# Kernel optimization log

Measured on AMD Instinct MI355X. Metric: run time of the kernel, lower is better.

## Reference

```python
import jax, jax.numpy as jnp
import numpy as np

L = 2          # loopnum
BS = 64        # batch
T = 512        # tracklength
EC = 1024      # ecnum
CA1 = 1024     # ca1num
CA3 = 1024     # ca3num
ACT = 2        # actnum
TS = 0.1
SIGMA = 5.0    # ca3sigma


def setup_inputs() -> dict:
    key = jax.random.key(0)
    ks = jax.random.split(key, 10)
    return {
        "cue_ec3input": jax.random.normal(ks[0], (BS, T, EC), dtype=jnp.float32),
        "ec3_last": jax.random.uniform(ks[1], (L, BS, EC), dtype=jnp.float32),
        "ec5_last": jax.random.uniform(ks[2], (L, BS, EC), dtype=jnp.float32),
        "ca1_last": jax.random.uniform(ks[3], (L, BS, CA1), dtype=jnp.float32),
        # per-loop parameters, stacked on leading loop axis (mirrors nn.ModuleList)
        "wca3ca1": jax.random.uniform(ks[4], (L, CA3, CA1), dtype=jnp.float32) * 0.01,
        "wec3ca1": jax.random.normal(ks[5], (L, EC, CA1), dtype=jnp.float32) * 0.03,   # ~xavier scale
        "wca1ec5": jax.random.normal(ks[6], (L, CA1, EC), dtype=jnp.float32) * 0.03,
        "ca1bias": jnp.zeros((L, CA1), dtype=jnp.float32),
        "ec5bias": jnp.zeros((L, EC), dtype=jnp.float32),
        # interLayer i: nn.Linear(ca1num, ecnum) -> weight (EC, CA1), bias (EC,)
        "inter_w": jax.random.normal(ks[7], (L, EC, CA1), dtype=jnp.float32) * 0.02,
        "inter_b": jnp.zeros((L, EC), dtype=jnp.float32),
        "wca1act": jax.random.normal(ks[8], (CA1, ACT), dtype=jnp.float32) * 0.03,
        "actbias": jnp.zeros((ACT,), dtype=jnp.float32),
    }


def reference(cue_ec3input, ec3_last, ec5_last, ca1_last,
              wca3ca1, wec3ca1, wca1ec5, ca1bias, ec5bias,
              inter_w, inter_b, wca1act, actbias):
    ca3center = jnp.linspace(0.0, float(T), CA3)          # (CA3,)
    positions = jnp.arange(T, dtype=jnp.float32)          # (T,)
    cue_t = jnp.swapaxes(cue_ec3input, 0, 1)              # (T, BS, EC)

    def step(carry, xin):
        ec3, ec5, ca1 = carry                             # each (L, BS, dim)
        x, cue_x = xin                                    # scalar, (BS, EC)
        ca3 = jnp.exp(-(ca3center - x) ** 2 / (2.0 * SIGMA ** 2))  # (CA3,)
        ec3input = cue_x
        new_ec3, new_ec5, new_ca1 = [], [], []
        for i in range(L):                                # fixed, structurally distinct loops
            ca1_i = jax.nn.relu(
                jax.nn.sigmoid(10.0 * (ca3 @ wca3ca1[i] - 0.5))           # (CA1,)
                * (1.0 + 3.0 * jax.nn.sigmoid(ec3[i] @ wec3ca1[i]))       # (BS, CA1)
                - ca1bias[i]
            )
            ec5_i = ec5[i] + 10.0 * TS * (ca1_i @ wca1ec5[i]) + ec5bias[i]
            ec5_i = 0.69 + 0.3 * jax.nn.sigmoid(4.0 * (ec5_i - 0.3))
            ec3_i = ec5_i * ec3[i] + 0.6 * ec3input
            ec3input = ca1_i @ inter_w[i].T + inter_b[i]  # feed next loop
            new_ec3.append(ec3_i); new_ec5.append(ec5_i); new_ca1.append(ca1_i)
        ec3 = jnp.stack(new_ec3); ec5 = jnp.stack(new_ec5); ca1 = jnp.stack(new_ca1)
        # histories record batch element 0 only, as in the original
        hist = (ec3[:, 0, :], ec5[:, 0, :], ca1[:, 0, :])
        return (ec3, ec5, ca1), hist

    (ec3, ec5, ca1), (ec3his, ec5his, ca1his) = jax.lax.scan(
        step, (ec3_last, ec5_last, ca1_last), (positions, cue_t))

    # scan stacks on axis 0 -> (T, L, dim); original layout is (L, T, dim)
    ec3his = jnp.swapaxes(ec3his, 0, 1)
    ec5his = jnp.swapaxes(ec5his, 0, 1)
    ca1his = jnp.swapaxes(ca1his, 0, 1)

    actCell = ca1[-1] @ wca1act + actbias                 # (BS, ACT)
    return actCell, ec3his, ec5his, ca1his
```

## Files before the change

kernel.cpp:

```cpp
#include <hip/hip_runtime.h>

#define Lnum 2
#define BSn  64
#define Tn   512
#define ECn  1024
#define CA1n 1024
#define CHUNK 16

typedef short bf16x8 __attribute__((ext_vector_type(8)));
typedef float f32x4  __attribute__((ext_vector_type(4)));

#define MFMA16(a,b,c) __builtin_amdgcn_mfma_f32_16x16x32_bf16((a),(b),(c),0,0,0)

#define OUT_E3  128
#define OUT_E5  (128 + Lnum*Tn*ECn)
#define OUT_CA1 (128 + 2*Lnum*Tn*ECn)

#define WS_FLAGS 0
#define WS_EC3S  8192
#define WS_CA1S  4202496
#define WS_EC5F  8396800
#define WS_EC3F  8921088
#define WS_CA1L  9445376
#define WS_S     9707520
#define WS_W1T   11804672
#define WS_W2T   15998976
#define WS_W3T   20193280

#define AST(p, v) __hip_atomic_store((p), (v), __ATOMIC_RELAXED, __HIP_MEMORY_SCOPE_AGENT)
#define ALD(p)    __hip_atomic_load((p), __ATOMIC_RELAXED, __HIP_MEMORY_SCOPE_AGENT)

__device__ __forceinline__ float sigm(float x) { return 1.0f / (1.0f + __expf(-x)); }

__device__ __forceinline__ unsigned f2bfu(float f) {
  unsigned u = __float_as_uint(f);
  u += 0x7fffu + ((u >> 16) & 1u);
  return u >> 16;
}
__device__ __forceinline__ short f2bf(float f) { return (short)f2bfu(f); }
__device__ __forceinline__ float bf2f(short s) {
  return __uint_as_float(((unsigned)(unsigned short)s) << 16);
}

__device__ __forceinline__ void pollCnt(const unsigned* c, unsigned need) {
  while (ALD(c) < need) __builtin_amdgcn_s_sleep(1);
  __builtin_amdgcn_sched_barrier(0);
  asm volatile("" ::: "memory");
}
__device__ __forceinline__ void pollCnt2(const unsigned* c0, const unsigned* c1,
                                         unsigned need) {
  while ((ALD(c0) < need) | (ALD(c1) < need)) __builtin_amdgcn_s_sleep(1);
  __builtin_amdgcn_sched_barrier(0);
  asm volatile("" ::: "memory");
}
__device__ __forceinline__ void publish(unsigned* c) {
  asm volatile("s_waitcnt vmcnt(0)" ::: "memory");
  __syncthreads();
  if (threadIdx.x == 0)
    __hip_atomic_fetch_add(c, 1u, __ATOMIC_RELAXED, __HIP_MEMORY_SCOPE_AGENT);
}


__global__ void prep_state(const float* __restrict__ ec3_last,
                           const float* __restrict__ ec5_last,
                           unsigned* __restrict__ flags, unsigned* __restrict__ ec3su,
                           float* __restrict__ ec5f, float* __restrict__ ec3f) {
  int i = blockIdx.x * blockDim.x + threadIdx.x;
  if (i < 2048) flags[i] = 0u;
  float v3 = ec3_last[i];
  ec3f[i] = v3;
  ec5f[i] = ec5_last[i];
  if (i < Lnum * BSn * 512) {
    float lo = ec3_last[2 * i], hi = ec3_last[2 * i + 1];
    ec3su[15 * 65536 + i] = f2bfu(lo) | (f2bfu(hi) << 16);
  }
}

__global__ void prep_wt(const float* __restrict__ w1, const float* __restrict__ w2,
                        short* __restrict__ w1t, short* __restrict__ w2t) {
  __shared__ float tile[64][65];
  const int b = blockIdx.x;
  const int m  = b >> 9;
  const int li = (b >> 8) & 1;
  const int kt = (b >> 4) & 15;
  const int ct = b & 15;
  const float* src = (m == 0 ? w1 : w2) + li * (1024 * 1024);
  short* dst = (m == 0 ? w1t : w2t) + li * (1024 * 1024);
#pragma unroll
  for (int i = 0; i < 16; ++i) {
    int idx = threadIdx.x + i * 256;
    int r = idx >> 6, c = idx & 63;
    tile[r][c] = src[(kt * 64 + r) * 1024 + ct * 64 + c];
  }
  __syncthreads();
#pragma unroll
  for (int i = 0; i < 16; ++i) {
    int idx = threadIdx.x + i * 256;
    int c = idx >> 6, r = idx & 63;
    dst[(ct * 64 + c) * 1024 + kt * 64 + r] = f2bf(tile[r][c]);
  }
}

__global__ void prep_w3(const float* __restrict__ inter_w, short* __restrict__ w3t) {
  int i = blockIdx.x * blockDim.x + threadIdx.x;
  w3t[i] = f2bf(inter_w[i]);
}

__global__ void prep_ca3(const float* __restrict__ wca3ca1, short* __restrict__ S) {
  const int t = blockIdx.x >> 1, li = blockIdx.x & 1;
  __shared__ float gauss[192];
  const float stepc = 512.0f / 1023.0f;
  const float tf = (float)t;
  int kmin = (int)floorf((tf - 40.0f) / stepc) - 1; if (kmin < 0) kmin = 0;
  int kmax = (int)ceilf((tf + 40.0f) / stepc) + 1;  if (kmax > 1023) kmax = 1023;
  int nw = kmax - kmin + 1;
  for (int j = threadIdx.x; j < nw; j += 256) {
    float d = (float)(kmin + j) * stepc - tf;
    gauss[j] = __expf(-d * d * 0.02f);
  }
  __syncthreads();
  const float* W = wca3ca1 + li * (1024 * 1024);
  for (int c = threadIdx.x; c < 1024; c += 256) {
    float s = 0.0f;
    for (int j = 0; j < nw; ++j) s += gauss[j] * W[(kmin + j) * 1024 + c];
    S[(li * Tn + t) * 1024 + c] = f2bf(sigm(10.0f * (s - 0.5f)));
  }
}

__global__ void __launch_bounds__(256, 1) stepchunk(
    const float* __restrict__ cue,
    const short* __restrict__ w1t, const short* __restrict__ w2t,
    const short* __restrict__ w3t, const short* __restrict__ stab,
    const float* __restrict__ ca1bias, const float* __restrict__ ec5bias,
    const float* __restrict__ interb,
    unsigned* __restrict__ flags, short* __restrict__ ec3s,
    short* __restrict__ ca1s, float* __restrict__ ec5f, float* __restrict__ ec3f,
    float* __restrict__ ca1l, float* __restrict__ out, int t0) {
  extern __shared__ short lds[];
  short* BT1 = lds;
  short* BT2 = lds + 16 * 1024;
  short* BT3 = lds + 32 * 1024;

  unsigned* cntA0 = flags;
  unsigned* cntA1 = flags + 16;
  unsigned* cntB0 = flags + 32;
  unsigned* cntB1 = flags + 48;
  unsigned* ec3su = (unsigned*)ec3s;
  unsigned* ca1su = (unsigned*)ca1s;

  const int b = blockIdx.x;
  const int li = b & 1;
  const int c0 = (b >> 1) << 4;
  const int tid = threadIdx.x;
  const int lane = tid & 63, wave = tid >> 6;
  const int fr = lane & 15, ks = lane >> 4;
  const int r0 = wave << 4;
  const int ccol = c0 + fr;

  unsigned* myCntA = li ? cntA1 : cntA0;
  unsigned* myCntB = li ? cntB1 : cntB0;

  {
    int cp = tid & 15;
    int k0 = (tid >> 4) << 6;
    int xm = (cp & 7) << 3;
    const short* s1 = w1t + li * 1048576 + (c0 + cp) * 1024;
    const short* s2 = w2t + li * 1048576 + (c0 + cp) * 1024;
#pragma unroll
    for (int j = 0; j < 8; ++j) {
      int k = k0 + j * 8;
      *(bf16x8*)(BT1 + cp * 1024 + (k ^ xm)) = *(const bf16x8*)(s1 + k);
      *(bf16x8*)(BT2 + cp * 1024 + (k ^ xm)) = *(const bf16x8*)(s2 + k);
    }
    if (li == 1) {
      const short* s3 = w3t + (c0 + cp) * 1024;
#pragma unroll
      for (int j = 0; j < 8; ++j) {
        int k = k0 + j * 8;
        *(bf16x8*)(BT3 + cp * 1024 + (k ^ xm)) = *(const bf16x8*)(s3 + k);
      }
    }
  }
  __syncthreads();

  const int xsw = (fr & 7) << 3;
  const short* B1 = BT1 + fr * 1024;
  const short* B2 = BT2 + fr * 1024;
  const short* B3 = BT3 + fr * 1024;

  const float cb  = ca1bias[li * 1024 + ccol];
  const float e5b = ec5bias[li * 1024 + ccol];
  const float ib0 = interb[1024 + ccol];

  float e5r[4], e3r[4];
#pragma unroll
  for (int r = 0; r < 4; ++r) {
    int sidx = li * 65536 + (r0 + ks * 4 + r) * 1024 + ccol;
    e5r[r] = ec5f[sidx];
    e3r[r] = ec3f[sidx];
  }

  bf16x8 ar[32], ar3[32];

  for (int tt = 0; tt < CHUNK; ++tt) {
    const int t = t0 + tt;
    const int rd = (tt + 15) & 15;

    f32x4 cvv;
    {
      if (wave == 0) pollCnt(myCntB, 64u * (unsigned)t);
      __syncthreads();
      const short* A1 = ec3s + ((rd * 2 + li) * 64 + (r0 + fr)) * 1024 + ks * 8;
#pragma unroll
      for (int kk = 0; kk < 16; ++kk) {
        ar[kk]      = *(const bf16x8*)(A1 + kk * 32);
        ar[16 + kk] = *(const bf16x8*)(A1 + 512 + kk * 32);
      }
      __builtin_amdgcn_sched_barrier(0);
      f32x4 a0 = {0.f,0.f,0.f,0.f}, a1 = {0.f,0.f,0.f,0.f};
#pragma unroll
      for (int kk = 0; kk < 16; ++kk) {
        a0 = MFMA16(ar[kk],      *(const bf16x8*)(B1 + ((kk * 32 + ks * 8) ^ xsw)),       a0);
        a1 = MFMA16(ar[16 + kk], *(const bf16x8*)(B1 + ((512 + kk * 32 + ks * 8) ^ xsw)), a1);
      }
      f32x4 acc = a0 + a1;
      const float g = bf2f(stab[(li * Tn + t) * 1024 + ccol]);
#pragma unroll
      for (int r = 0; r < 4; ++r) {
        int grow = r0 + ks * 4 + r;
        float cv = fmaxf(g * (1.0f + 3.0f * sigm(acc[r])) - cb, 0.0f);
        cvv[r] = cv;
        unsigned my = f2bfu(cv);
        unsigned pr = (unsigned)__shfl_xor((int)my, 1);
        if ((fr & 1) == 0)
          AST(ca1su + ((tt * 2 + li) * 64 + grow) * 512 + ((c0 + fr) >> 1), my | (pr << 16));
      }
      publish(myCntA);
#pragma unroll
      for (int r = 0; r < 4; ++r) {
        int grow = r0 + ks * 4 + r;
        if (grow == 0) out[OUT_CA1 + (li * Tn + t) * 1024 + ccol] = cvv[r];
        if (t == Tn - 1 && li == 1) ca1l[grow * 1024 + ccol] = cvv[r];
      }
    }

    {
      float cueq[4];
      if (li == 0) {
#pragma unroll
        for (int r = 0; r < 4; ++r)
          cueq[r] = cue[((r0 + ks * 4 + r) * Tn + t) * 1024 + ccol];
      }
      if (wave == 0) {
        if (li == 0) pollCnt(cntA0, 64u * (unsigned)(t + 1));
        else         pollCnt2(cntA0, cntA1, 64u * (unsigned)(t + 1));
      }
      __syncthreads();
      const short* A2 = ca1s + ((tt * 2 + li) * 64 + (r0 + fr)) * 1024 + ks * 8;
#pragma unroll
      for (int kk = 0; kk < 16; ++kk) {
        ar[kk]      = *(const bf16x8*)(A2 + kk * 32);
        ar[16 + kk] = *(const bf16x8*)(A2 + 512 + kk * 32);
      }
      if (li == 1) {
        const short* A3 = ca1s + ((tt * 2) * 64 + (r0 + fr)) * 1024 + ks * 8;
#pragma unroll
        for (int kk = 0; kk < 16; ++kk) {
          ar3[kk]      = *(const bf16x8*)(A3 + kk * 32);
          ar3[16 + kk] = *(const bf16x8*)(A3 + 512 + kk * 32);
        }
      }
      __builtin_amdgcn_sched_barrier(0);
      f32x4 p0 = {0.f,0.f,0.f,0.f}, p1 = {0.f,0.f,0.f,0.f};
#pragma unroll
      for (int kk = 0; kk < 16; ++kk) {
        p0 = MFMA16(ar[kk],      *(const bf16x8*)(B2 + ((kk * 32 + ks * 8) ^ xsw)),       p0);
        p1 = MFMA16(ar[16 + kk], *(const bf16x8*)(B2 + ((512 + kk * 32 + ks * 8) ^ xsw)), p1);
      }
      f32x4 g2 = p0 + p1;

      f32x4 xin;
      if (li == 1) {
        f32x4 q0 = {0.f,0.f,0.f,0.f}, q1 = {0.f,0.f,0.f,0.f};
#pragma unroll
        for (int kk = 0; kk < 16; ++kk) {
          q0 = MFMA16(ar3[kk],      *(const bf16x8*)(B3 + ((kk * 32 + ks * 8) ^ xsw)),       q0);
          q1 = MFMA16(ar3[16 + kk], *(const bf16x8*)(B3 + ((512 + kk * 32 + ks * 8) ^ xsw)), q1);
        }
        f32x4 q = q0 + q1;
#pragma unroll
        for (int r = 0; r < 4; ++r) xin[r] = q[r] + ib0;
      } else {
#pragma unroll
        for (int r = 0; r < 4; ++r) xin[r] = cueq[r];
      }

#pragma unroll
      for (int r = 0; r < 4; ++r) {
        float raw = e5r[r] + g2[r] + e5b;
        float e5 = 0.69f + 0.3f * sigm(4.0f * (raw - 0.3f));
        e5r[r] = e5;
        float e3 = e5 * e3r[r] + 0.6f * xin[r];
        e3r[r] = e3;
        int grow = r0 + ks * 4 + r;
        unsigned my = f2bfu(e3);
        unsigned pr = (unsigned)__shfl_xor((int)my, 1);
        if ((fr & 1) == 0)
          AST(ec3su + ((tt * 2 + li) * 64 + grow) * 512 + ((c0 + fr) >> 1), my | (pr << 16));
      }
      publish(myCntB);
#pragma unroll
      for (int r = 0; r < 4; ++r) {
        int grow = r0 + ks * 4 + r;
        if (grow == 0) {
          out[OUT_E5 + (li * Tn + t) * 1024 + ccol] = e5r[r];
          out[OUT_E3 + (li * Tn + t) * 1024 + ccol] = e3r[r];
        }
      }
    }
  }

#pragma unroll
  for (int r = 0; r < 4; ++r) {
    int sidx = li * 65536 + (r0 + ks * 4 + r) * 1024 + ccol;
    ec5f[sidx] = e5r[r];
    ec3f[sidx] = e3r[r];
  }
}

__global__ void act_cell(const float* __restrict__ ca1l, const float* __restrict__ wca1act,
                         const float* __restrict__ actbias, float* __restrict__ out) {
  int tid = threadIdx.x;
  if (tid < 128) {
    int b = tid >> 1, a = tid & 1;
    float s = 0.0f;
    for (int k = 0; k < 1024; ++k) s += ca1l[b * 1024 + k] * wca1act[k * 2 + a];
    out[b * 2 + a] = s + actbias[a];
  }
}

extern "C" void kernel_launch(void* const* d_in, const int* in_sizes, int n_in,
                              void* d_out, int out_size, void* d_ws, size_t ws_size,
                              hipStream_t stream) {
  (void)in_sizes; (void)n_in; (void)out_size; (void)ws_size;
  const float* cue      = (const float*)d_in[0];
  const float* ec3_last = (const float*)d_in[1];
  const float* ec5_last = (const float*)d_in[2];
  const float* wca3ca1  = (const float*)d_in[4];
  const float* wec3ca1  = (const float*)d_in[5];
  const float* wca1ec5  = (const float*)d_in[6];
  const float* ca1bias  = (const float*)d_in[7];
  const float* ec5bias  = (const float*)d_in[8];
  const float* inter_w  = (const float*)d_in[9];
  const float* inter_b  = (const float*)d_in[10];
  const float* wca1act  = (const float*)d_in[11];
  const float* actbias  = (const float*)d_in[12];
  float* out = (float*)d_out;

  char* ws = (char*)d_ws;
  unsigned* flags = (unsigned*)(ws + WS_FLAGS);
  short* ec3s = (short*)(ws + WS_EC3S);
  short* ca1s = (short*)(ws + WS_CA1S);
  float* ec5f = (float*)(ws + WS_EC5F);
  float* ec3f = (float*)(ws + WS_EC3F);
  float* ca1l = (float*)(ws + WS_CA1L);
  short* stab = (short*)(ws + WS_S);
  short* w1t  = (short*)(ws + WS_W1T);
  short* w2t  = (short*)(ws + WS_W2T);
  short* w3t  = (short*)(ws + WS_W3T);

  prep_state<<<dim3(512), dim3(256), 0, stream>>>(ec3_last, ec5_last, flags,
                                                  (unsigned*)ec3s, ec5f, ec3f);
  prep_wt<<<dim3(1024), dim3(256), 0, stream>>>(wec3ca1, wca1ec5, w1t, w2t);
  prep_w3<<<dim3(4096), dim3(256), 0, stream>>>(inter_w, w3t);
  prep_ca3<<<dim3(1024), dim3(256), 0, stream>>>(wca3ca1, stab);

  hipFuncSetAttribute((const void*)stepchunk,
                      hipFuncAttributeMaxDynamicSharedMemorySize, 98304);

  for (int c = 0; c < Tn / CHUNK; ++c) {
    stepchunk<<<dim3(128), dim3(256), 98304, stream>>>(
        cue, w1t, w2t, w3t, stab, ca1bias, ec5bias, inter_b,
        flags, ec3s, ca1s, ec5f, ec3f, ca1l, out, c * CHUNK);
  }

  act_cell<<<dim3(1), dim3(128), 0, stream>>>(ca1l, wca1act, actbias, out);
}
```

Before: 8.144 ms.

## Spread step-chunk blocks across XCDs, stage stores via LDS, add mirror counter

Launches 512 blocks and keeps only those with blockIdx&7 < 2, so the 128 active blocks land on specific XCDs. The apparent goal is to keep each loop's blocks together and reduce cross-die coherence traffic for the flag polling. Per-step ca1/ec3 tiles are staged through LDS and written as packed 64-bit stores. Loop 1 now waits on a separate mirror counter that loop 0 bumps, and loop 0 stores its ca1 tile a second time before that bump. W3 is read from global memory instead of LDS, which cuts dynamic LDS and allows two blocks per CU. History outputs are buffered in LDS and written once per chunk. The risk is extra global reads for W3 and wasted launches of idle blocks.

New measurement: 16.68 ms. 105% more time.

```diff
diff --git a/kernel.cpp b/kernel.cpp
--- a/kernel.cpp
+++ b/kernel.cpp
@@ -27,8 +27,10 @@
 #define WS_W2T   15998976
 #define WS_W3T   20193280
 
-#define AST(p, v) __hip_atomic_store((p), (v), __ATOMIC_RELAXED, __HIP_MEMORY_SCOPE_AGENT)
+#define AST64(p, v) __hip_atomic_store((p), (v), __ATOMIC_RELAXED, __HIP_MEMORY_SCOPE_AGENT)
+#define AADD(p, v) __hip_atomic_fetch_add((p), (v), __ATOMIC_RELAXED, __HIP_MEMORY_SCOPE_AGENT)
 #define ALD(p)    __hip_atomic_load((p), __ATOMIC_RELAXED, __HIP_MEMORY_SCOPE_AGENT)
+#define ASTU(p, v) __hip_atomic_store((p), (v), __ATOMIC_RELAXED, __HIP_MEMORY_SCOPE_AGENT)
 
 __device__ __forceinline__ float sigm(float x) { return 1.0f / (1.0f + __expf(-x)); }
 
@@ -53,11 +55,9 @@
   __builtin_amdgcn_sched_barrier(0);
   asm volatile("" ::: "memory");
 }
-__device__ __forceinline__ void publish(unsigned* c) {
+__device__ __forceinline__ void drainSync() {
   asm volatile("s_waitcnt vmcnt(0)" ::: "memory");
   __syncthreads();
-  if (threadIdx.x == 0)
-    __hip_atomic_fetch_add(c, 1u, __ATOMIC_RELAXED, __HIP_MEMORY_SCOPE_AGENT);
 }
 
 
@@ -72,7 +72,7 @@
   ec5f[i] = ec5_last[i];
   if (i < Lnum * BSn * 512) {
     float lo = ec3_last[2 * i], hi = ec3_last[2 * i + 1];
-    ec3su[15 * 65536 + i] = f2bfu(lo) | (f2bfu(hi) << 16);
+    ASTU(ec3su + 15 * 65536 + i, f2bfu(lo) | (f2bfu(hi) << 16));
   }
 }
 
@@ -127,7 +127,7 @@
   }
 }
 
-__global__ void __launch_bounds__(256, 1) stepchunk(
+__global__ void __launch_bounds__(256, 2) stepchunk(
     const float* __restrict__ cue,
     const short* __restrict__ w1t, const short* __restrict__ w2t,
     const short* __restrict__ w3t, const short* __restrict__ stab,
@@ -137,25 +137,30 @@
     short* __restrict__ ca1s, float* __restrict__ ec5f, float* __restrict__ ec3f,
     float* __restrict__ ca1l, float* __restrict__ out, int t0) {
   extern __shared__ short lds[];
+  const int b = blockIdx.x;
+  const int li = b & 7;
+  if (li >= Lnum) return;
+
   short* BT1 = lds;
   short* BT2 = lds + 16 * 1024;
-  short* BT3 = lds + 32 * 1024;
+  float* hist = (float*)(lds + 32 * 1024);
+  short* XP   = lds + 32 * 1024 + 1536;
 
   unsigned* cntA0 = flags;
-  unsigned* cntA1 = flags + 16;
-  unsigned* cntB0 = flags + 32;
+  unsigned* cntB0 = flags + 16;
+  unsigned* cntA1 = flags + 32;
   unsigned* cntB1 = flags + 48;
-  unsigned* ec3su = (unsigned*)ec3s;
-  unsigned* ca1su = (unsigned*)ca1s;
-
-  const int b = blockIdx.x;
-  const int li = b & 1;
-  const int c0 = (b >> 1) << 4;
+  unsigned* cntM  = flags + 64;
+
+  const int wid = b >> 3;
+  const int c0 = wid << 4;
   const int tid = threadIdx.x;
   const int lane = tid & 63, wave = tid >> 6;
   const int fr = lane & 15, ks = lane >> 4;
   const int r0 = wave << 4;
   const int ccol = c0 + fr;
+  const int rw = lane >> 2, j = lane & 3;
+  short* XPw = XP + wave * 256;
 
   unsigned* myCntA = li ? cntA1 : cntA0;
   unsigned* myCntB = li ? cntB1 : cntB0;
@@ -167,26 +172,18 @@
     const short* s1 = w1t + li * 1048576 + (c0 + cp) * 1024;
     const short* s2 = w2t + li * 1048576 + (c0 + cp) * 1024;
 #pragma unroll
-    for (int j = 0; j < 8; ++j) {
-      int k = k0 + j * 8;
+    for (int jj = 0; jj < 8; ++jj) {
+      int k = k0 + jj * 8;
       *(bf16x8*)(BT1 + cp * 1024 + (k ^ xm)) = *(const bf16x8*)(s1 + k);
       *(bf16x8*)(BT2 + cp * 1024 + (k ^ xm)) = *(const bf16x8*)(s2 + k);
     }
-    if (li == 1) {
-      const short* s3 = w3t + (c0 + cp) * 1024;
-#pragma unroll
-      for (int j = 0; j < 8; ++j) {
-        int k = k0 + j * 8;
-        *(bf16x8*)(BT3 + cp * 1024 + (k ^ xm)) = *(const bf16x8*)(s3 + k);
-      }
-    }
   }
   __syncthreads();
 
   const int xsw = (fr & 7) << 3;
   const short* B1 = BT1 + fr * 1024;
   const short* B2 = BT2 + fr * 1024;
-  const short* B3 = BT3 + fr * 1024;
+  const short* W3 = w3t + ccol * 1024 + ks * 8;
 
   const float cb  = ca1bias[li * 1024 + ccol];
   const float e5b = ec5bias[li * 1024 + ccol];
@@ -200,13 +197,17 @@
     e3r[r] = ec3f[sidx];
   }
 
-  bf16x8 ar[32], ar3[32];
+  bf16x8 ar[32];
+  f32x4 cvv;
+  unsigned long long mirv = 0ull;
+  int mirIdx = 0;
+  unsigned long long* ca1q = (unsigned long long*)ca1s;
+  unsigned long long* ec3q = (unsigned long long*)ec3s;
 
   for (int tt = 0; tt < CHUNK; ++tt) {
     const int t = t0 + tt;
     const int rd = (tt + 15) & 15;
 
-    f32x4 cvv;
     {
       if (wave == 0) pollCnt(myCntB, 64u * (unsigned)t);
       __syncthreads();
@@ -227,24 +228,21 @@
       const float g = bf2f(stab[(li * Tn + t) * 1024 + ccol]);
 #pragma unroll
       for (int r = 0; r < 4; ++r) {
-        int grow = r0 + ks * 4 + r;
         float cv = fmaxf(g * (1.0f + 3.0f * sigm(acc[r])) - cb, 0.0f);
         cvv[r] = cv;
-        unsigned my = f2bfu(cv);
-        unsigned pr = (unsigned)__shfl_xor((int)my, 1);
-        if ((fr & 1) == 0)
-          AST(ca1su + ((tt * 2 + li) * 64 + grow) * 512 + ((c0 + fr) >> 1), my | (pr << 16));
-      }
-      publish(myCntA);
-#pragma unroll
-      for (int r = 0; r < 4; ++r) {
-        int grow = r0 + ks * 4 + r;
-        if (grow == 0) out[OUT_CA1 + (li * Tn + t) * 1024 + ccol] = cvv[r];
-        if (t == Tn - 1 && li == 1) ca1l[grow * 1024 + ccol] = cvv[r];
-      }
+        XPw[(ks * 4 + r) * 16 + fr] = f2bf(cv);
+      }
+      if (wave == 0 && ks == 0) hist[tt * 16 + fr] = cvv[0];
+      unsigned long long pk = *(const unsigned long long*)(XPw + rw * 16 + j * 4);
+      int idx = ((tt * 2 + li) * 64 + r0 + rw) * 256 + (c0 >> 2) + j;
+      ca1q[idx] = pk;
+      if (li == 0) { mirv = pk; mirIdx = idx; }
+      drainSync();
+      if (tid == 0) AADD(myCntA, 1u);
     }
 
     {
+      if (li == 0) AST64(ca1q + mirIdx, mirv);
       float cueq[4];
       if (li == 0) {
 #pragma unroll
@@ -253,7 +251,7 @@
       }
       if (wave == 0) {
         if (li == 0) pollCnt(cntA0, 64u * (unsigned)(t + 1));
-        else         pollCnt2(cntA0, cntA1, 64u * (unsigned)(t + 1));
+        else         pollCnt2(cntA1, cntM, 64u * (unsigned)(t + 1));
       }
       __syncthreads();
       const short* A2 = ca1s + ((tt * 2 + li) * 64 + (r0 + fr)) * 1024 + ks * 8;
@@ -262,14 +260,6 @@
         ar[kk]      = *(const bf16x8*)(A2 + kk * 32);
         ar[16 + kk] = *(const bf16x8*)(A2 + 512 + kk * 32);
       }
-      if (li == 1) {
-        const short* A3 = ca1s + ((tt * 2) * 64 + (r0 + fr)) * 1024 + ks * 8;
-#pragma unroll
-        for (int kk = 0; kk < 16; ++kk) {
-          ar3[kk]      = *(const bf16x8*)(A3 + kk * 32);
-          ar3[16 + kk] = *(const bf16x8*)(A3 + 512 + kk * 32);
-        }
-      }
       __builtin_amdgcn_sched_barrier(0);
       f32x4 p0 = {0.f,0.f,0.f,0.f}, p1 = {0.f,0.f,0.f,0.f};
 #pragma unroll
@@ -281,11 +271,18 @@
 
       f32x4 xin;
       if (li == 1) {
+        const short* A3 = ca1s + ((tt * 2) * 64 + (r0 + fr)) * 1024 + ks * 8;
+#pragma unroll
+        for (int kk = 0; kk < 16; ++kk) {
+          ar[kk]      = *(const bf16x8*)(A3 + kk * 32);
+          ar[16 + kk] = *(const bf16x8*)(A3 + 512 + kk * 32);
+        }
+        __builtin_amdgcn_sched_barrier(0);
         f32x4 q0 = {0.f,0.f,0.f,0.f}, q1 = {0.f,0.f,0.f,0.f};
 #pragma unroll
         for (int kk = 0; kk < 16; ++kk) {
-          q0 = MFMA16(ar3[kk],      *(const bf16x8*)(B3 + ((kk * 32 + ks * 8) ^ xsw)),       q0);
-          q1 = MFMA16(ar3[16 + kk], *(const bf16x8*)(B3 + ((512 + kk * 32 + ks * 8) ^ xsw)), q1);
+          q0 = MFMA16(ar[kk],      *(const bf16x8*)(W3 + kk * 32),       q0);
+          q1 = MFMA16(ar[16 + kk], *(const bf16x8*)(W3 + 512 + kk * 32), q1);
         }
         f32x4 q = q0 + q1;
 #pragma unroll
@@ -302,24 +299,35 @@
         e5r[r] = e5;
         float e3 = e5 * e3r[r] + 0.6f * xin[r];
         e3r[r] = e3;
-        int grow = r0 + ks * 4 + r;
-        unsigned my = f2bfu(e3);
-        unsigned pr = (unsigned)__shfl_xor((int)my, 1);
-        if ((fr & 1) == 0)
-          AST(ec3su + ((tt * 2 + li) * 64 + grow) * 512 + ((c0 + fr) >> 1), my | (pr << 16));
-      }
-      publish(myCntB);
-#pragma unroll
-      for (int r = 0; r < 4; ++r) {
-        int grow = r0 + ks * 4 + r;
-        if (grow == 0) {
-          out[OUT_E5 + (li * Tn + t) * 1024 + ccol] = e5r[r];
-          out[OUT_E3 + (li * Tn + t) * 1024 + ccol] = e3r[r];
-        }
+        XPw[(ks * 4 + r) * 16 + fr] = f2bf(e3);
+      }
+      if (wave == 0 && ks == 0) {
+        hist[256 + tt * 16 + fr] = e5r[0];
+        hist[512 + tt * 16 + fr] = e3r[0];
+      }
+      unsigned long long pk3 = *(const unsigned long long*)(XPw + rw * 16 + j * 4);
+      ec3q[((tt * 2 + li) * 64 + r0 + rw) * 256 + (c0 >> 2) + j] = pk3;
+      drainSync();
+      if (tid == 0) {
+        AADD(myCntB, 1u);
+        if (li == 0) AADD(cntM, 1u);
       }
     }
   }
 
+  if (wave == 0) {
+    for (int s = ks; s < CHUNK; s += 4) {
+      int t = t0 + s;
+      out[OUT_CA1 + (li * Tn + t) * 1024 + c0 + fr] = hist[s * 16 + fr];
+      out[OUT_E5  + (li * Tn + t) * 1024 + c0 + fr] = hist[256 + s * 16 + fr];
+      out[OUT_E3  + (li * Tn + t) * 1024 + c0 + fr] = hist[512 + s * 16 + fr];
+    }
+  }
+  if (t0 + CHUNK == Tn && li == 1) {
+#pragma unroll
+    for (int r = 0; r < 4; ++r)
+      ca1l[(r0 + ks * 4 + r) * 1024 + ccol] = cvv[r];
+  }
 #pragma unroll
   for (int r = 0; r < 4; ++r) {
     int sidx = li * 65536 + (r0 + ks * 4 + r) * 1024 + ccol;
@@ -376,10 +384,10 @@
   prep_ca3<<<dim3(1024), dim3(256), 0, stream>>>(wca3ca1, stab);
 
   hipFuncSetAttribute((const void*)stepchunk,
-                      hipFuncAttributeMaxDynamicSharedMemorySize, 98304);
+                      hipFuncAttributeMaxDynamicSharedMemorySize, 70656);
 
   for (int c = 0; c < Tn / CHUNK; ++c) {
-    stepchunk<<<dim3(128), dim3(256), 98304, stream>>>(
+    stepchunk<<<dim3(512), dim3(256), 70656, stream>>>(
         cue, w1t, w2t, w3t, stab, ca1bias, ec5bias, inter_b,
         flags, ec3s, ca1s, ec5f, ec3f, ca1l, out, c * CHUNK);
   }
```
